# Performance work log

Hardware: AMD Instinct MI355X
Metric: run time of the kernel (lower is better)

The kernel has to match this reference:

```python
import jax, jax.numpy as jnp
import numpy as np

B, S, D, H = 4, 2048, 512, 8
DK = D // H

def setup_inputs() -> dict:
    key = jax.random.key(0)
    ks = jax.random.split(key, 16)
    inp = {
        "query": jax.random.normal(ks[0], (B, S, D), dtype=jnp.float32),
        "key": jax.random.normal(ks[1], (B, S, D), dtype=jnp.float32),
        "value": jax.random.normal(ks[2], (B, S, D), dtype=jnp.float32),
        "mask": jnp.ones((B, 1, 1, S), dtype=jnp.int32),
        "is_organic": jax.random.uniform(ks[3], (B, S), dtype=jnp.float32),
        # torch nn.Linear params: y = x @ W.T + b
        "Wq": jax.random.normal(ks[4], (D, D), dtype=jnp.float32) * (1.0 / np.sqrt(D)),
        "bq": jnp.zeros((D,), dtype=jnp.float32),
        "Wk": jax.random.normal(ks[5], (D, D), dtype=jnp.float32) * (1.0 / np.sqrt(D)),
        "bk": jnp.zeros((D,), dtype=jnp.float32),
        "Wv": jax.random.normal(ks[6], (D, D), dtype=jnp.float32) * (1.0 / np.sqrt(D)),
        "bv": jnp.zeros((D,), dtype=jnp.float32),
        "Wo": jax.random.normal(ks[7], (D, D), dtype=jnp.float32) * (1.0 / np.sqrt(D)),
        "bo": jnp.zeros((D,), dtype=jnp.float32),
        "Worg": jax.random.normal(ks[8], (H, 1), dtype=jnp.float32),
        "borg": jnp.zeros((H,), dtype=jnp.float32),
    }
    return inp

def reference(query, key, value, mask, is_organic, Wq, bq, Wk, bk, Wv, bv, Wo, bo, Worg, borg):
    # Project and split heads: [B,S,D] -> [B,H,S,DK]
    def heads(x, W, b):
        return (x @ W.T + b).reshape(B, S, H, DK).transpose(0, 2, 1, 3)
    Q = heads(query, Wq, bq)
    K = heads(key, Wk, bk)
    V = heads(value, Wv, bv)
    # Scaled scores [B,H,S,S]
    scores = jnp.einsum('bhqd,bhkd->bhqk', Q, K) / jnp.sqrt(jnp.float32(DK))
    # Organic bias: Linear(1->H) on is_organic -> [B,S,H] -> [B,H,S,1], added per query row
    organic = is_organic[..., None] @ Worg.T + borg          # [B,S,H]
    scores = scores + organic.transpose(0, 2, 1)[..., None]  # [B,H,S,1]
    scores = jnp.where(mask == 0, jnp.float32(-1e9), scores)
    attention = jax.nn.softmax(scores, axis=-1)  # dropout is identity in eval
    context = jnp.einsum('bhqk,bhkd->bhqd', attention, V)
    context = context.transpose(0, 2, 1, 3).reshape(B, S, D)
    output = context @ Wo.T + bo
    return output, attention
```

## Files before the change

### kernel.cpp

```cpp
#include <hip/hip_runtime.h>
#include <cstdint>
#include <cstddef>


static constexpr int B  = 4;
static constexpr int S  = 2048;
static constexpr int D  = 512;
static constexpr int H  = 8;
static constexpr int DK = 64;
static constexpr int N  = B * S;
static constexpr int BH = B * H;

__device__ __forceinline__ float f4c(const float4& v, int j) {
  return j == 0 ? v.x : j == 1 ? v.y : j == 2 ? v.z : v.w;
}

__device__ __forceinline__ void fma4x4(float (&acc)[4][4], const float4 a, const float4 b) {
  const float av[4] = {a.x, a.y, a.z, a.w};
  const float bv[4] = {b.x, b.y, b.z, b.w};
#pragma unroll
  for (int i = 0; i < 4; ++i)
#pragma unroll
    for (int j = 0; j < 4; ++j) acc[i][j] = fmaf(av[i], bv[j], acc[i][j]);
}

__global__ __launch_bounds__(256, 4) void proj_kernel(
    const float* __restrict__ X, const float* __restrict__ W,
    const float* __restrict__ bias, float* __restrict__ Y, int head_layout)
{
  __shared__ float As[32][64];
  __shared__ float Bs[32][128];
  const int tid = threadIdx.x;
  const int tx = tid & 15, ty = tid >> 4;
  const int row0 = blockIdx.x * 64, col0 = blockIdx.y * 128;

  const int brq = (tid & 31) * 4;
  const int bcq = (tid >> 5) * 4;
  const int arq = (tid & 15) * 4;
  const int acq = ((tid >> 4) & 7) * 4;

  float acc[2][4][4] = {};
  const int ra = ty * 4, ca = tx * 4;

  for (int kc = 0; kc < D; kc += 32) {
    float4 wr[4], xr[4];
#pragma unroll
    for (int rr = 0; rr < 4; ++rr)
      wr[rr] = *(const float4*)&W[(size_t)(col0 + brq + rr) * D + kc + bcq];
    if (tid < 128) {
#pragma unroll
      for (int rr = 0; rr < 4; ++rr)
        xr[rr] = *(const float4*)&X[(size_t)(row0 + arq + rr) * D + kc + acq];
    }
    __syncthreads();
#pragma unroll
    for (int j = 0; j < 4; ++j)
      *(float4*)&Bs[bcq + j][brq] =
          make_float4(f4c(wr[0], j), f4c(wr[1], j), f4c(wr[2], j), f4c(wr[3], j));
    if (tid < 128) {
#pragma unroll
      for (int j = 0; j < 4; ++j)
        *(float4*)&As[acq + j][arq] =
            make_float4(f4c(xr[0], j), f4c(xr[1], j), f4c(xr[2], j), f4c(xr[3], j));
    }
    __syncthreads();
#pragma unroll 4
    for (int k = 0; k < 32; ++k) {
      const float4 av = *(const float4*)&As[k][ra];
      const float4 b0 = *(const float4*)&Bs[k][ca];
      const float4 b1 = *(const float4*)&Bs[k][64 + ca];
      fma4x4(acc[0], av, b0);
      fma4x4(acc[1], av, b1);
    }
  }

  const int oc0 = col0 + ca;
  const float4 bi0 = *(const float4*)&bias[oc0];
  const float4 bi1 = *(const float4*)&bias[oc0 + 64];
#pragma unroll
  for (int i = 0; i < 4; ++i) {
    const int row = row0 + ra + i;
    const int bb = row >> 11, ss = row & (S - 1);
#pragma unroll
    for (int oh = 0; oh < 2; ++oh) {
      const int oc = oc0 + oh * 64;
      size_t dst;
      if (head_layout) {
        dst = ((size_t)(bb * H + (oc >> 6)) * S + ss) * DK + (oc & 63);
      } else {
        dst = (size_t)row * D + oc;
      }
      const float4 bi = oh ? bi1 : bi0;
      *(float4*)&Y[dst] = make_float4(acc[oh][i][0] + bi.x, acc[oh][i][1] + bi.y,
                                      acc[oh][i][2] + bi.z, acc[oh][i][3] + bi.w);
    }
  }
}

__global__ __launch_bounds__(256, 2) void scores_kernel(
    const float* __restrict__ Q, const float* __restrict__ Kp,
    const int* __restrict__ mask, float* __restrict__ attn)
{
  __shared__ float Qs[64][128];
  __shared__ float Ks[64][128];
  const int tid = threadIdx.x;
  const int tx = tid & 15, ty = tid >> 4;
  const int q0 = blockIdx.x * 128, k0 = blockIdx.y * 128;
  const int bh = (int)blockIdx.z, b = bh >> 3;
  const float* __restrict__ Qh = Q + (size_t)bh * S * DK;
  const float* __restrict__ Kh = Kp + (size_t)bh * S * DK;

  const int rq4 = (tid & 31) * 4;
  const int ch  = (tid >> 5) * 4;
#pragma unroll
  for (int half = 0; half < 64; half += 32) {
    const int cd4 = ch + half;
    float4 qr[4], kr[4];
#pragma unroll
    for (int rr = 0; rr < 4; ++rr) {
      qr[rr] = *(const float4*)&Qh[(size_t)(q0 + rq4 + rr) * DK + cd4];
      kr[rr] = *(const float4*)&Kh[(size_t)(k0 + rq4 + rr) * DK + cd4];
    }
#pragma unroll
    for (int j = 0; j < 4; ++j) {
      *(float4*)&Qs[cd4 + j][rq4] =
          make_float4(f4c(qr[0], j), f4c(qr[1], j), f4c(qr[2], j), f4c(qr[3], j));
      *(float4*)&Ks[cd4 + j][rq4] =
          make_float4(f4c(kr[0], j), f4c(kr[1], j), f4c(kr[2], j), f4c(kr[3], j));
    }
  }
  __syncthreads();

  float acc[2][2][4][4] = {};
  const int qa = ty * 4, ka = tx * 4;
#pragma unroll 8
  for (int d = 0; d < 64; ++d) {
    const float4 a0 = *(const float4*)&Qs[d][qa];
    const float4 a1 = *(const float4*)&Qs[d][64 + qa];
    const float4 b0 = *(const float4*)&Ks[d][ka];
    const float4 b1 = *(const float4*)&Ks[d][64 + ka];
    fma4x4(acc[0][0], a0, b0); fma4x4(acc[0][1], a0, b1);
    fma4x4(acc[1][0], a1, b0); fma4x4(acc[1][1], a1, b1);
  }

  int mk[2][4];
#pragma unroll
  for (int kh = 0; kh < 2; ++kh)
#pragma unroll
    for (int j = 0; j < 4; ++j)
      mk[kh][j] = mask[b * S + k0 + kh * 64 + ka + j];

#pragma unroll
  for (int qh = 0; qh < 2; ++qh)
#pragma unroll
    for (int i = 0; i < 4; ++i) {
      const int q = q0 + qh * 64 + qa + i;
      float* __restrict__ dst = &attn[((size_t)bh * S + q) * S + k0];
#pragma unroll
      for (int kh = 0; kh < 2; ++kh) {
        float4 st;
        st.x = mk[kh][0] ? acc[qh][kh][i][0] * 0.125f : -1e9f;
        st.y = mk[kh][1] ? acc[qh][kh][i][1] * 0.125f : -1e9f;
        st.z = mk[kh][2] ? acc[qh][kh][i][2] * 0.125f : -1e9f;
        st.w = mk[kh][3] ? acc[qh][kh][i][3] * 0.125f : -1e9f;
        *(float4*)&dst[kh * 64 + ka] = st;
      }
    }
}

__global__ __launch_bounds__(256) void mlreduce_kernel(
    const float* __restrict__ attn, float* __restrict__ Mrow, float* __restrict__ Linv)
{
  const int row = (int)blockIdx.x;
  const float* __restrict__ p = attn + (size_t)row * S;
  const int tid = threadIdx.x;
  const float4 a = *(const float4*)&p[tid * 4];
  const float4 c = *(const float4*)&p[1024 + tid * 4];

  float m = fmaxf(fmaxf(fmaxf(a.x, a.y), fmaxf(a.z, a.w)),
                  fmaxf(fmaxf(c.x, c.y), fmaxf(c.z, c.w)));
#pragma unroll
  for (int off = 32; off > 0; off >>= 1) m = fmaxf(m, __shfl_xor(m, off));
  __shared__ float redm[4], reds[4];
  const int wv = tid >> 6, ln = tid & 63;
  if (ln == 0) redm[wv] = m;
  __syncthreads();
  m = fmaxf(fmaxf(redm[0], redm[1]), fmaxf(redm[2], redm[3]));

  float s = __expf(a.x - m) + __expf(a.y - m) + __expf(a.z - m) + __expf(a.w - m)
          + __expf(c.x - m) + __expf(c.y - m) + __expf(c.z - m) + __expf(c.w - m);
#pragma unroll
  for (int off = 32; off > 0; off >>= 1) s += __shfl_xor(s, off);
  if (ln == 0) reds[wv] = s;
  __syncthreads();
  if (tid == 0) {
    const float l = reds[0] + reds[1] + reds[2] + reds[3];
    Mrow[row] = m;
    Linv[row] = 1.0f / l;
  }
}

__global__ __launch_bounds__(256, 3) void context_kernel(
    float* __restrict__ attn, const float* __restrict__ V,
    const float* __restrict__ Mrow, const float* __restrict__ Linv,
    float* __restrict__ C)
{
  __shared__ float Ps[64][128];
  __shared__ float Vs[64][64];
  const int tid = threadIdx.x;
  const int tx = tid & 15, ty = tid >> 4;
  const int q0 = blockIdx.x * 128;
  const int bh = (int)blockIdx.z, b = bh >> 3, h = bh & 7;
  float* __restrict__ A = attn + (size_t)bh * S * S;
  const float* __restrict__ Vh = V + (size_t)bh * S * DK;

  const int rq4 = (tid & 31) * 4;
  const int ch  = (tid >> 5) * 4;
  float mr[4], il[4];
#pragma unroll
  for (int rr = 0; rr < 4; ++rr) {
    mr[rr] = Mrow[(size_t)bh * S + q0 + rq4 + rr];
    il[rr] = Linv[(size_t)bh * S + q0 + rq4 + rr];
  }

  float acc[2][4][4] = {};
  const int qa = ty * 4, da = tx * 4;

  for (int k0 = 0; k0 < S; k0 += 64) {
    __syncthreads();
#pragma unroll
    for (int half = 0; half < 64; half += 32) {
      const int cd4 = ch + half;
      float4 pr[4];
#pragma unroll
      for (int rr = 0; rr < 4; ++rr) {
        float* __restrict__ ap = &A[(size_t)(q0 + rq4 + rr) * S + k0 + cd4];
        float4 v = *(const float4*)ap;
        v.x = __expf(v.x - mr[rr]) * il[rr];
        v.y = __expf(v.y - mr[rr]) * il[rr];
        v.z = __expf(v.z - mr[rr]) * il[rr];
        v.w = __expf(v.w - mr[rr]) * il[rr];
        *(float4*)ap = v;
        pr[rr] = v;
      }
#pragma unroll
      for (int j = 0; j < 4; ++j)
        *(float4*)&Ps[cd4 + j][rq4] =
            make_float4(f4c(pr[0], j), f4c(pr[1], j), f4c(pr[2], j), f4c(pr[3], j));
    }
#pragma unroll
    for (int jj = 0; jj < 4; ++jj) {
      const int r = ty + 16 * jj;
      *(float4*)&Vs[r][da] = *(const float4*)&Vh[(size_t)(k0 + r) * DK + da];
    }
    __syncthreads();
#pragma unroll 8
    for (int k = 0; k < 64; ++k) {
      const float4 a0 = *(const float4*)&Ps[k][qa];
      const float4 a1 = *(const float4*)&Ps[k][64 + qa];
      const float4 bv = *(const float4*)&Vs[k][da];
      fma4x4(acc[0], a0, bv);
      fma4x4(acc[1], a1, bv);
    }
  }

#pragma unroll
  for (int qh = 0; qh < 2; ++qh)
#pragma unroll
    for (int i = 0; i < 4; ++i) {
      const int q = q0 + qh * 64 + qa + i;
      *(float4*)&C[((size_t)(b * S + q)) * D + h * DK + da] =
          make_float4(acc[qh][i][0], acc[qh][i][1], acc[qh][i][2], acc[qh][i][3]);
    }
}

extern "C" void kernel_launch(void* const* d_in, const int* in_sizes, int n_in,
                              void* d_out, int out_size, void* d_ws, size_t ws_size,
                              hipStream_t stream)
{
  (void)in_sizes; (void)n_in; (void)out_size; (void)ws_size;
  const float* query = (const float*)d_in[0];
  const float* key   = (const float*)d_in[1];
  const float* value = (const float*)d_in[2];
  const int*   mask  = (const int*)d_in[3];
  const float* Wq = (const float*)d_in[5];
  const float* bq = (const float*)d_in[6];
  const float* Wk = (const float*)d_in[7];
  const float* bk = (const float*)d_in[8];
  const float* Wv = (const float*)d_in[9];
  const float* bv = (const float*)d_in[10];
  const float* Wo = (const float*)d_in[11];
  const float* bo = (const float*)d_in[12];

  float* out  = (float*)d_out;
  float* attn = out + (size_t)N * D;

  float* Qb = (float*)d_ws;
  float* Kb = Qb + (size_t)N * D;
  float* Vb = Kb + (size_t)N * D;
  float* Cb = Vb + (size_t)N * D;

  float* Mrow = out;
  float* Linv = out + (size_t)BH * S;

  const dim3 blk(256);
  proj_kernel<<<dim3(N / 64, D / 128), blk, 0, stream>>>(query, Wq, bq, Qb, 1);
  proj_kernel<<<dim3(N / 64, D / 128), blk, 0, stream>>>(key,   Wk, bk, Kb, 1);
  proj_kernel<<<dim3(N / 64, D / 128), blk, 0, stream>>>(value, Wv, bv, Vb, 1);
  scores_kernel<<<dim3(S / 128, S / 128, BH), blk, 0, stream>>>(Qb, Kb, mask, attn);
  mlreduce_kernel<<<dim3(BH * S), blk, 0, stream>>>(attn, Mrow, Linv);
  context_kernel<<<dim3(S / 128, 1, BH), blk, 0, stream>>>(attn, Vb, Mrow, Linv, Cb);
  proj_kernel<<<dim3(N / 64, D / 128), blk, 0, stream>>>(Cb, Wo, bo, out, 0);
}
```

Measured before the change: 1.428 ms.

## Use split-bf16 MFMA for scores and fuse partial softmax stats into scores kernel

```diff
diff --git a/kernel.cpp b/kernel.cpp
--- a/kernel.cpp
+++ b/kernel.cpp
@@ -10,6 +10,10 @@
 static constexpr int DK = 64;
 static constexpr int N  = B * S;
 static constexpr int BH = B * H;
+static constexpr int KT = S / 128;
+
+typedef __bf16 bf16x8 __attribute__((ext_vector_type(8)));
+typedef float  f32x16 __attribute__((ext_vector_type(16)));
 
 __device__ __forceinline__ float f4c(const float4& v, int j) {
   return j == 0 ? v.x : j == 1 ? v.y : j == 2 ? v.z : v.w;
@@ -24,9 +28,16 @@
     for (int j = 0; j < 4; ++j) acc[i][j] = fmaf(av[i], bv[j], acc[i][j]);
 }
 
+__device__ __forceinline__ ushort f2bf(float x) {
+  uint32_t u = __float_as_uint(x);
+  u += 0x7FFFu + ((u >> 16) & 1u);
+  return (ushort)(u >> 16);
+}
+
 __global__ __launch_bounds__(256, 4) void proj_kernel(
     const float* __restrict__ X, const float* __restrict__ W,
-    const float* __restrict__ bias, float* __restrict__ Y, int head_layout)
+    const float* __restrict__ bias, float* __restrict__ Yf,
+    ushort* __restrict__ Yhi, ushort* __restrict__ Ylo, int mode)
 {
   __shared__ float As[32][64];
   __shared__ float Bs[32][128];
@@ -84,120 +95,147 @@
 #pragma unroll
     for (int oh = 0; oh < 2; ++oh) {
       const int oc = oc0 + oh * 64;
-      size_t dst;
-      if (head_layout) {
-        dst = ((size_t)(bb * H + (oc >> 6)) * S + ss) * DK + (oc & 63);
+      const float4 bi = oh ? bi1 : bi0;
+      float v[4] = {acc[oh][i][0] + bi.x, acc[oh][i][1] + bi.y,
+                    acc[oh][i][2] + bi.z, acc[oh][i][3] + bi.w};
+      if (mode == 0) {
+        *(float4*)&Yf[(size_t)row * D + oc] = make_float4(v[0], v[1], v[2], v[3]);
       } else {
-        dst = (size_t)row * D + oc;
+        const size_t dst = ((size_t)(bb * H + (oc >> 6)) * S + ss) * DK + (oc & 63);
+        if (mode == 1) {
+          *(float4*)&Yf[dst] = make_float4(v[0], v[1], v[2], v[3]);
+        } else {
+          ushort h[4], lo[4];
+#pragma unroll
+          for (int j = 0; j < 4; ++j) {
+            h[j] = f2bf(v[j]);
+            const float hf = __uint_as_float((uint32_t)h[j] << 16);
+            lo[j] = f2bf(v[j] - hf);
+          }
+          *(ushort4*)&Yhi[dst] = make_ushort4(h[0], h[1], h[2], h[3]);
+          *(ushort4*)&Ylo[dst] = make_ushort4(lo[0], lo[1], lo[2], lo[3]);
+        }
       }
-      const float4 bi = oh ? bi1 : bi0;
-      *(float4*)&Y[dst] = make_float4(acc[oh][i][0] + bi.x, acc[oh][i][1] + bi.y,
-                                      acc[oh][i][2] + bi.z, acc[oh][i][3] + bi.w);
     }
   }
 }
 
 __global__ __launch_bounds__(256, 2) void scores_kernel(
-    const float* __restrict__ Q, const float* __restrict__ Kp,
-    const int* __restrict__ mask, float* __restrict__ attn)
-{
-  __shared__ float Qs[64][128];
-  __shared__ float Ks[64][128];
+    const ushort* __restrict__ Qh, const ushort* __restrict__ Ql,
+    const ushort* __restrict__ Kh, const ushort* __restrict__ Kl,
+    const int* __restrict__ mask, float* __restrict__ attn,
+    float* __restrict__ Mp, float* __restrict__ Lp)
+{
+  __shared__ ushort sQh[128 * 64], sQl[128 * 64];
+  __shared__ ushort sKh[128 * 64], sKl[128 * 64];
   const int tid = threadIdx.x;
-  const int tx = tid & 15, ty = tid >> 4;
   const int q0 = blockIdx.x * 128, k0 = blockIdx.y * 128;
   const int bh = (int)blockIdx.z, b = bh >> 3;
-  const float* __restrict__ Qh = Q + (size_t)bh * S * DK;
-  const float* __restrict__ Kh = Kp + (size_t)bh * S * DK;
-
-  const int rq4 = (tid & 31) * 4;
-  const int ch  = (tid >> 5) * 4;
-#pragma unroll
-  for (int half = 0; half < 64; half += 32) {
-    const int cd4 = ch + half;
-    float4 qr[4], kr[4];
-#pragma unroll
-    for (int rr = 0; rr < 4; ++rr) {
-      qr[rr] = *(const float4*)&Qh[(size_t)(q0 + rq4 + rr) * DK + cd4];
-      kr[rr] = *(const float4*)&Kh[(size_t)(k0 + rq4 + rr) * DK + cd4];
-    }
-#pragma unroll
-    for (int j = 0; j < 4; ++j) {
-      *(float4*)&Qs[cd4 + j][rq4] =
-          make_float4(f4c(qr[0], j), f4c(qr[1], j), f4c(qr[2], j), f4c(qr[3], j));
-      *(float4*)&Ks[cd4 + j][rq4] =
-          make_float4(f4c(kr[0], j), f4c(kr[1], j), f4c(kr[2], j), f4c(kr[3], j));
-    }
-  }
+
+  auto stage = [&](const ushort* __restrict__ src, ushort* dst) {
+#pragma unroll
+    for (int i = tid; i < 1024; i += 256) {
+      const int row = i >> 3, kg = i & 7;
+      const float4 v = *(const float4*)&src[(size_t)row * DK + kg * 8];
+      *(float4*)((char*)dst + ((row * 128 + kg * 16) ^ ((row & 7) << 4))) = v;
+    }
+  };
+  stage(Qh + ((size_t)bh * S + q0) * DK, sQh);
+  stage(Ql + ((size_t)bh * S + q0) * DK, sQl);
+  stage(Kh + ((size_t)bh * S + k0) * DK, sKh);
+  stage(Kl + ((size_t)bh * S + k0) * DK, sKl);
   __syncthreads();
 
-  float acc[2][2][4][4] = {};
-  const int qa = ty * 4, ka = tx * 4;
-#pragma unroll 8
-  for (int d = 0; d < 64; ++d) {
-    const float4 a0 = *(const float4*)&Qs[d][qa];
-    const float4 a1 = *(const float4*)&Qs[d][64 + qa];
-    const float4 b0 = *(const float4*)&Ks[d][ka];
-    const float4 b1 = *(const float4*)&Ks[d][64 + ka];
-    fma4x4(acc[0][0], a0, b0); fma4x4(acc[0][1], a0, b1);
-    fma4x4(acc[1][0], a1, b0); fma4x4(acc[1][1], a1, b1);
-  }
-
-  int mk[2][4];
-#pragma unroll
-  for (int kh = 0; kh < 2; ++kh)
-#pragma unroll
-    for (int j = 0; j < 4; ++j)
-      mk[kh][j] = mask[b * S + k0 + kh * 64 + ka + j];
-
-#pragma unroll
-  for (int qh = 0; qh < 2; ++qh)
-#pragma unroll
-    for (int i = 0; i < 4; ++i) {
-      const int q = q0 + qh * 64 + qa + i;
-      float* __restrict__ dst = &attn[((size_t)bh * S + q) * S + k0];
-#pragma unroll
-      for (int kh = 0; kh < 2; ++kh) {
-        float4 st;
-        st.x = mk[kh][0] ? acc[qh][kh][i][0] * 0.125f : -1e9f;
-        st.y = mk[kh][1] ? acc[qh][kh][i][1] * 0.125f : -1e9f;
-        st.z = mk[kh][2] ? acc[qh][kh][i][2] * 0.125f : -1e9f;
-        st.w = mk[kh][3] ? acc[qh][kh][i][3] * 0.125f : -1e9f;
-        *(float4*)&dst[kh * 64 + ka] = st;
+  const int wid = tid >> 6, lane = tid & 63;
+  const int wm = wid >> 1, wn = wid & 1;
+  const int g = lane >> 5, l31 = lane & 31;
+
+  f32x16 acc[2][2] = {};
+#pragma unroll
+  for (int ks = 0; ks < 4; ++ks) {
+    const int kb = (ks * 2 + g) * 16;
+    bf16x8 aH[2], aL[2], bHf[2], bLf[2];
+#pragma unroll
+    for (int mq = 0; mq < 2; ++mq) {
+      const int row = wm * 64 + mq * 32 + l31;
+      const int byo = (row * 128 + kb) ^ ((row & 7) << 4);
+      aH[mq] = *(const bf16x8*)((const char*)sQh + byo);
+      aL[mq] = *(const bf16x8*)((const char*)sQl + byo);
+    }
+#pragma unroll
+    for (int nq = 0; nq < 2; ++nq) {
+      const int row = wn * 64 + nq * 32 + l31;
+      const int byo = (row * 128 + kb) ^ ((row & 7) << 4);
+      bHf[nq] = *(const bf16x8*)((const char*)sKh + byo);
+      bLf[nq] = *(const bf16x8*)((const char*)sKl + byo);
+    }
+#pragma unroll
+    for (int mq = 0; mq < 2; ++mq)
+#pragma unroll
+      for (int nq = 0; nq < 2; ++nq) {
+        acc[mq][nq] = __builtin_amdgcn_mfma_f32_32x32x16_bf16(aH[mq], bHf[nq], acc[mq][nq], 0, 0, 0);
+        acc[mq][nq] = __builtin_amdgcn_mfma_f32_32x32x16_bf16(aH[mq], bLf[nq], acc[mq][nq], 0, 0, 0);
+        acc[mq][nq] = __builtin_amdgcn_mfma_f32_32x32x16_bf16(aL[mq], bHf[nq], acc[mq][nq], 0, 0, 0);
       }
-    }
+  }
+
+  const int c0 = k0 + wn * 64 + l31;
+  const int mk0 = mask[b * S + c0];
+  const int mk1 = mask[b * S + c0 + 32];
+  float* sm = (float*)sQh;
+  float* sl = sm + 256;
+  __syncthreads();
+
+#pragma unroll
+  for (int mq = 0; mq < 2; ++mq) {
+#pragma unroll
+    for (int reg = 0; reg < 16; ++reg) {
+      const int rloc = wm * 64 + mq * 32 + (reg & 3) + 8 * (reg >> 2) + 4 * g;
+      const float v0 = mk0 ? acc[mq][0][reg] * 0.125f : -1e9f;
+      const float v1 = mk1 ? acc[mq][1][reg] * 0.125f : -1e9f;
+      float* dst = &attn[((size_t)bh * S + q0 + rloc) * S + (k0 + wn * 64) + l31];
+      dst[0]  = v0;
+      dst[32] = v1;
+      float m = fmaxf(v0, v1);
+#pragma unroll
+      for (int off = 16; off > 0; off >>= 1) m = fmaxf(m, __shfl_xor(m, off));
+      float e = __expf(v0 - m) + __expf(v1 - m);
+#pragma unroll
+      for (int off = 16; off > 0; off >>= 1) e += __shfl_xor(e, off);
+      if (l31 == 0) { sm[rloc * 2 + wn] = m; sl[rloc * 2 + wn] = e; }
+    }
+  }
+  __syncthreads();
+  if (tid < 128) {
+    const float m0 = sm[tid * 2], m1 = sm[tid * 2 + 1];
+    const float l0 = sl[tid * 2], l1 = sl[tid * 2 + 1];
+    const float m = fmaxf(m0, m1);
+    const float l = l0 * __expf(m0 - m) + l1 * __expf(m1 - m);
+    const size_t pr = ((size_t)bh * S + q0 + tid) * KT + blockIdx.y;
+    Mp[pr] = m;
+    Lp[pr] = l;
+  }
 }
 
 __global__ __launch_bounds__(256) void mlreduce_kernel(
-    const float* __restrict__ attn, float* __restrict__ Mrow, float* __restrict__ Linv)
-{
-  const int row = (int)blockIdx.x;
-  const float* __restrict__ p = attn + (size_t)row * S;
-  const int tid = threadIdx.x;
-  const float4 a = *(const float4*)&p[tid * 4];
-  const float4 c = *(const float4*)&p[1024 + tid * 4];
-
-  float m = fmaxf(fmaxf(fmaxf(a.x, a.y), fmaxf(a.z, a.w)),
-                  fmaxf(fmaxf(c.x, c.y), fmaxf(c.z, c.w)));
-#pragma unroll
-  for (int off = 32; off > 0; off >>= 1) m = fmaxf(m, __shfl_xor(m, off));
-  __shared__ float redm[4], reds[4];
-  const int wv = tid >> 6, ln = tid & 63;
-  if (ln == 0) redm[wv] = m;
-  __syncthreads();
-  m = fmaxf(fmaxf(redm[0], redm[1]), fmaxf(redm[2], redm[3]));
-
-  float s = __expf(a.x - m) + __expf(a.y - m) + __expf(a.z - m) + __expf(a.w - m)
-          + __expf(c.x - m) + __expf(c.y - m) + __expf(c.z - m) + __expf(c.w - m);
-#pragma unroll
-  for (int off = 32; off > 0; off >>= 1) s += __shfl_xor(s, off);
-  if (ln == 0) reds[wv] = s;
-  __syncthreads();
-  if (tid == 0) {
-    const float l = reds[0] + reds[1] + reds[2] + reds[3];
-    Mrow[row] = m;
-    Linv[row] = 1.0f / l;
-  }
+    const float* __restrict__ Mp, const float* __restrict__ Lp,
+    float* __restrict__ Mrow, float* __restrict__ Linv)
+{
+  const int r = (int)blockIdx.x * 256 + threadIdx.x;
+  float mp[KT], lp[KT];
+#pragma unroll
+  for (int i = 0; i < KT / 4; ++i) {
+    *(float4*)&mp[i * 4] = *(const float4*)&Mp[(size_t)r * KT + i * 4];
+    *(float4*)&lp[i * 4] = *(const float4*)&Lp[(size_t)r * KT + i * 4];
+  }
+  float m = mp[0];
+#pragma unroll
+  for (int i = 1; i < KT; ++i) m = fmaxf(m, mp[i]);
+  float l = 0.0f;
+#pragma unroll
+  for (int i = 0; i < KT; ++i) l += lp[i] * __expf(mp[i] - m);
+  Mrow[r] = m;
+  Linv[r] = 1.0f / l;
 }
 
 __global__ __launch_bounds__(256, 3) void context_kernel(
@@ -295,20 +333,24 @@
   float* out  = (float*)d_out;
   float* attn = out + (size_t)N * D;
 
-  float* Qb = (float*)d_ws;
-  float* Kb = Qb + (size_t)N * D;
-  float* Vb = Kb + (size_t)N * D;
-  float* Cb = Vb + (size_t)N * D;
-
-  float* Mrow = out;
-  float* Linv = out + (size_t)BH * S;
+  ushort* Qh = (ushort*)d_ws;
+  ushort* Ql = Qh + (size_t)N * D;
+  ushort* Kh = Ql + (size_t)N * D;
+  ushort* Kl = Kh + (size_t)N * D;
+  float*  Vb = (float*)(Kl + (size_t)N * D);
+  float*  Cb = Vb + (size_t)N * D;
+
+  float* Mp   = out;
+  float* Lp   = Mp + (size_t)BH * S * KT;
+  float* Mrow = Lp + (size_t)BH * S * KT;
+  float* Linv = Mrow + (size_t)BH * S;
 
   const dim3 blk(256);
-  proj_kernel<<<dim3(N / 64, D / 128), blk, 0, stream>>>(query, Wq, bq, Qb, 1);
-  proj_kernel<<<dim3(N / 64, D / 128), blk, 0, stream>>>(key,   Wk, bk, Kb, 1);
-  proj_kernel<<<dim3(N / 64, D / 128), blk, 0, stream>>>(value, Wv, bv, Vb, 1);
-  scores_kernel<<<dim3(S / 128, S / 128, BH), blk, 0, stream>>>(Qb, Kb, mask, attn);
-  mlreduce_kernel<<<dim3(BH * S), blk, 0, stream>>>(attn, Mrow, Linv);
+  proj_kernel<<<dim3(N / 64, D / 128), blk, 0, stream>>>(query, Wq, bq, nullptr, Qh, Ql, 2);
+  proj_kernel<<<dim3(N / 64, D / 128), blk, 0, stream>>>(key,   Wk, bk, nullptr, Kh, Kl, 2);
+  proj_kernel<<<dim3(N / 64, D / 128), blk, 0, stream>>>(value, Wv, bv, Vb, nullptr, nullptr, 1);
+  scores_kernel<<<dim3(S / 128, S / 128, BH), blk, 0, stream>>>(Qh, Ql, Kh, Kl, mask, attn, Mp, Lp);
+  mlreduce_kernel<<<dim3(BH * S / 256), blk, 0, stream>>>(Mp, Lp, Mrow, Linv);
   context_kernel<<<dim3(S / 128, 1, BH), blk, 0, stream>>>(attn, Vb, Mrow, Linv, Cb);
-  proj_kernel<<<dim3(N / 64, D / 128), blk, 0, stream>>>(Cb, Wo, bo, out, 0);
-}
+  proj_kernel<<<dim3(N / 64, D / 128), blk, 0, stream>>>(Cb, Wo, bo, out, nullptr, nullptr, 0);
+}
```

After: 1.427 ms. Within noise of the previous version (-0.1%).
